# Optimization experiments

Hardware: AMD Instinct MI355X
Metric: run time of the kernel (lower is better)

The kernel has to match this reference:

```python
import jax, jax.numpy as jnp
import numpy as np

SIGMAS = [15, 80, 250]  # hardcoded defaults in retinex_MSR


def _gauss_k1d(sigma):
    # matches get_gauss_kernel(sigma, dim=1)
    ksize = int(np.floor(sigma * 6) / 2) * 2 + 1
    k = np.arange(ksize, dtype=np.float32) - ksize // 2
    k = np.exp(-k ** 2 / (2.0 * sigma ** 2))
    k /= k.sum()
    return jnp.asarray(k)


def _gauss_blur(x, k1d):
    # x: (N, 1, H, W); separable blur with zero padding, same as F.conv2d
    K = k1d.shape[0]
    pad = K // 2
    dn = ('NCHW', 'OIHW', 'NCHW')
    kv = k1d.reshape(1, 1, K, 1)
    kh = k1d.reshape(1, 1, 1, K)
    x = jax.lax.conv_general_dilated(x, kv, (1, 1), [(pad, pad), (0, 0)], dimension_numbers=dn)
    x = jax.lax.conv_general_dilated(x, kh, (1, 1), [(0, 0), (pad, pad)], dimension_numbers=dn)
    return x


def setup_inputs() -> dict:
    key = jax.random.key(0)
    img = jax.random.uniform(key, (16, 3, 512, 512), dtype=jnp.float32)
    return {"img": img}


def reference(img):
    B, C, H, W = img.shape
    # all channels processed identically as single-channel depthwise convs:
    # fold channels into batch for one big conv per sigma
    x = img.astype(jnp.float32).reshape(B * C, 1, H, W)
    w = 1.0 / len(SIGMAS)  # default equal weights summing to 1
    r = jnp.zeros((B * C, 1, H, W), dtype=jnp.float32)
    for sigma in SIGMAS:
        r = r + jnp.log(_gauss_blur(x, _gauss_k1d(sigma)) + 1.0) * w
    r = r.reshape(B, C, H, W)
    # per-channel min-max stretch, global over batch and spatial dims
    mmin = r.min(axis=(0, 2, 3), keepdims=True)
    mmax = r.max(axis=(0, 2, 3), keepdims=True)
    return (r - mmin) / (mmax - mmin)
```

## Files before the change

kernel.cpp:

```cpp
#include <hip/hip_runtime.h>
#include <math.h>


#define NSL 48

#define W0_OFF 0
#define W1_OFF 512
#define W2_OFF 1280
#define MM_OFF 2816
#define G16_BYTE_OFF 16384
#define X16_BYTE_OFF 1589248
#define T16_BYTE_OFF 26755072

typedef _Float16 half8 __attribute__((ext_vector_type(8)));
typedef float f32x4 __attribute__((ext_vector_type(4)));

__device__ __forceinline__ void gload16(const void* g, void* l) {
  __builtin_amdgcn_global_load_lds(
      (const __attribute__((address_space(1))) void*)g,
      (__attribute__((address_space(3))) void*)l, 16, 0, 0);
}

#define WAITV3() asm volatile("s_waitcnt vmcnt(3)" ::: "memory")
#define WAITV0() asm volatile("s_waitcnt vmcnt(0)" ::: "memory")
#define SCHEDB() __builtin_amdgcn_sched_barrier(0)
#define BARRIER() __builtin_amdgcn_s_barrier()

__global__ void wkern(float* __restrict__ ws) {
  __shared__ float red[256];
  const int s = blockIdx.x;
  const int Ks[3] = {91, 481, 1501};
  const float sg[3] = {15.f, 80.f, 250.f};
  const int off[3] = {W0_OFF, W1_OFF, W2_OFF};
  const int alloc[3] = {512, 768, 1536};
  const int K = Ks[s], A = alloc[s];
  float* wb = ws + off[s];
  const int t = threadIdx.x;
  for (int i = t; i < A; i += 256) wb[i] = 0.f;
  __syncthreads();
  const float inv2s2 = 1.f / (2.f * sg[s] * sg[s]);
  float part = 0.f;
  for (int i = t; i < K; i += 256) {
    const float d = (float)(i - K / 2);
    const float e = __expf(-d * d * inv2s2);
    wb[16 + i] = e;
    part += e;
  }
  red[t] = part;
  __syncthreads();
  for (int st = 128; st > 0; st >>= 1) {
    if (t < st) red[t] += red[t + st];
    __syncthreads();
  }
  const float inv = 1.f / red[0];
  for (int i = t; i < K; i += 256) wb[16 + i] *= inv;
}

__global__ void mm_init(unsigned* __restrict__ mm) {
  const int t = threadIdx.x;
  if (t < 3) mm[t] = 0xFFFFFFFFu;
  else if (t < 6) mm[t] = 0u;
}

__global__ void gkern(const float* __restrict__ ws, _Float16* __restrict__ gb) {
  const int y = blockIdx.x;
  const int s = blockIdx.y;
  const int Rs[3] = {45, 240, 750};
  const int off[3] = {W0_OFF, W1_OFF, W2_OFF};
  const float* w = ws + off[s] + 16;
  _Float16* g = gb + ((size_t)s << 18) + ((size_t)y << 9);
  const int R = Rs[s], K = 2 * R + 1;
  for (int x = threadIdx.x; x < 512; x += 256) {
    const int i = x - y + R;
    const float v = (i >= 0 && i < K) ? w[i] : 0.f;
    g[x] = (_Float16)v;
  }
}

__global__ __launch_bounds__(256) void xconv(const float* __restrict__ X,
                                             _Float16* __restrict__ X16) {
  const size_t i = ((size_t)blockIdx.x * 256 + threadIdx.x) << 3;
  const float4 v0 = *reinterpret_cast<const float4*>(X + i);
  const float4 v1 = *reinterpret_cast<const float4*>(X + i + 4);
  half8 h;
  h[0] = (_Float16)v0.x; h[1] = (_Float16)v0.y;
  h[2] = (_Float16)v0.z; h[3] = (_Float16)v0.w;
  h[4] = (_Float16)v1.x; h[5] = (_Float16)v1.y;
  h[6] = (_Float16)v1.z; h[7] = (_Float16)v1.w;
  *reinterpret_cast<half8*>(X16 + i) = h;
}

#define STAGE_P(buf)                                 \
  do {                                               \
    gload16(pA0, &As[buf][t << 3]);                  \
    gload16(pA1, &As[buf][(256 + t) << 3]);          \
    gload16(pB0, &Bs[buf][t << 3]);                  \
    pA0 += 32; pA1 += 32; pB0 += 32;                 \
  } while (0)

#define FRAGS_AND_MFMA(buf)                                                         \
  do {                                                                              \
    half8 af[4], bf[2];                                                             \
    _Pragma("unroll") for (int f = 0; f < 4; ++f)                                   \
        af[f] = *reinterpret_cast<const half8*>(                                    \
            &As[buf][(((wr << 6) + (f << 4) + lr) << 5) + (lg << 3)]);              \
    _Pragma("unroll") for (int f = 0; f < 2; ++f)                                   \
        bf[f] = *reinterpret_cast<const half8*>(                                    \
            &Bs[buf][(((wc << 5) + (f << 4) + lr) << 5) + (lg << 3)]);              \
    _Pragma("unroll") for (int fm = 0; fm < 4; ++fm)                                \
        _Pragma("unroll") for (int fn = 0; fn < 2; ++fn)                            \
        acc[fm][fn] = __builtin_amdgcn_mfma_f32_16x16x32_f16(af[fm], bf[fn],        \
                                                             acc[fm][fn], 0, 0, 0); \
  } while (0)

#define K_PIPELINE_LOOP()                                                           \
  do {                                                                              \
    const _Float16* pA0 =                                                           \
        Ap + ((size_t)(bm + (t >> 2)) << 9) + (klo << 5) + ((t & 3) << 3);          \
    const _Float16* pA1 = pA0 + ((size_t)64 << 9);                                  \
    const _Float16* pB0 =                                                           \
        Bp + ((size_t)(bn + (t >> 2)) << 9) + (klo << 5) + ((t & 3) << 3);          \
    STAGE_P(0);                                                                     \
    STAGE_P(1);                                                                     \
    int cb = 0;                                                                     \
    for (int kt = klo; kt <= khi; ++kt) {                                           \
      if (kt < khi) { WAITV3(); } else { WAITV0(); }                                \
      SCHEDB();                                                                     \
      BARRIER();                                                                    \
      SCHEDB();                                                                     \
      if (kt + 2 <= khi) {                                                          \
        const int sb = (cb + 2 >= 3) ? cb - 1 : cb + 2;                             \
        STAGE_P(sb);                                                                \
      }                                                                             \
      FRAGS_AND_MFMA(cb);                                                           \
      cb = (cb == 2) ? 0 : cb + 1;                                                  \
    }                                                                               \
  } while (0)

__global__ __launch_bounds__(256, 4) void gemm1_k(const _Float16* __restrict__ X16,
                                                  const _Float16* __restrict__ G16,
                                                  _Float16* __restrict__ T16) {
  __shared__ __align__(16) _Float16 As[3][128 * 32];
  __shared__ __align__(16) _Float16 Bs[3][64 * 32];
  const int t = threadIdx.x;
  const int lane = t & 63, wave = t >> 6;
  const int wr = wave >> 1, wc = wave & 1;
  const int lr = lane & 15, lg = lane >> 4;
  const int bn = blockIdx.x << 6;
  const int bm = blockIdx.y << 7;
  const int z = blockIdx.z;
  const int s = z / NSL;
  const int slice = z - s * NSL;
  const int Rs[3] = {45, 240, 750};
  const int R = Rs[s];
  const _Float16* Ap = G16 + ((size_t)s << 18);
  const _Float16* Bp = X16 + ((size_t)slice << 18);
  _Float16* Tout = T16 + ((size_t)z << 18);

  int klo = bm - R;
  klo = (klo > 0 ? klo : 0) >> 5;
  int khi = bm + 127 + R;
  if (khi > 511) khi = 511;
  khi >>= 5;

  f32x4 acc[4][2];
#pragma unroll
  for (int i = 0; i < 4; ++i)
#pragma unroll
    for (int j = 0; j < 2; ++j) acc[i][j] = (f32x4){0.f, 0.f, 0.f, 0.f};

  K_PIPELINE_LOOP();

#pragma unroll
  for (int fm = 0; fm < 4; ++fm)
#pragma unroll
    for (int fn = 0; fn < 2; ++fn) {
      const int a0 = bm + (wr << 6) + (fm << 4) + (lg << 2);
      const int b0 = bn + (wc << 5) + (fn << 4) + lr;
#pragma unroll
      for (int j = 0; j < 4; ++j)
        Tout[((size_t)(a0 + j) << 9) + b0] = (_Float16)acc[fm][fn][j];
    }
}

__global__ __launch_bounds__(256, 3) void gemm2_k(const _Float16* __restrict__ G16,
                                                  const _Float16* __restrict__ T16,
                                                  float* __restrict__ out,
                                                  unsigned* __restrict__ mm) {
  __shared__ __align__(16) _Float16 As[3][128 * 32];
  __shared__ __align__(16) _Float16 Bs[3][64 * 32];
  __shared__ float smn[4], smx[4];
  const int t = threadIdx.x;
  const int lane = t & 63, wave = t >> 6;
  const int wr = wave >> 1, wc = wave & 1;
  const int lr = lane & 15, lg = lane >> 4;
  const int bn = blockIdx.x << 6;
  const int bm = blockIdx.y << 7;
  const int slice = blockIdx.z;
  const float w3 = 1.f / 3.f;
  const int Rs[3] = {45, 240, 750};

  f32x4 res[4][2];
#pragma unroll
  for (int i = 0; i < 4; ++i)
#pragma unroll
    for (int j = 0; j < 2; ++j) res[i][j] = (f32x4){0.f, 0.f, 0.f, 0.f};

#pragma unroll 1
  for (int s = 0; s < 3; ++s) {
    const int R = Rs[s];
    const _Float16* Ap = G16 + ((size_t)s << 18);
    const _Float16* Bp = T16 + ((size_t)(s * NSL + slice) << 18);
    int klo = bm - R;
    klo = (klo > 0 ? klo : 0) >> 5;
    int khi = bm + 127 + R;
    if (khi > 511) khi = 511;
    khi >>= 5;

    f32x4 acc[4][2];
#pragma unroll
    for (int i = 0; i < 4; ++i)
#pragma unroll
      for (int j = 0; j < 2; ++j) acc[i][j] = (f32x4){0.f, 0.f, 0.f, 0.f};

    BARRIER();
    K_PIPELINE_LOOP();

#pragma unroll
    for (int fm = 0; fm < 4; ++fm)
#pragma unroll
      for (int fn = 0; fn < 2; ++fn)
#pragma unroll
        for (int j = 0; j < 4; ++j)
          res[fm][fn][j] += w3 * __logf(acc[fm][fn][j] + 1.f);
  }

  float mn = 3.4e38f, mx = -3.4e38f;
#pragma unroll
  for (int fm = 0; fm < 4; ++fm)
#pragma unroll
    for (int fn = 0; fn < 2; ++fn) {
      const int rb = bm + (wr << 6) + (fm << 4) + (lg << 2);
      const int cg = bn + (wc << 5) + (fn << 4) + lr;
      float* op = out + ((size_t)slice << 18) + ((size_t)rb << 9) + cg;
#pragma unroll
      for (int j = 0; j < 4; ++j) {
        const float v = res[fm][fn][j];
        op[j << 9] = v;
        mn = fminf(mn, v);
        mx = fmaxf(mx, v);
      }
    }
#pragma unroll
  for (int off = 32; off > 0; off >>= 1) {
    mn = fminf(mn, __shfl_xor(mn, off));
    mx = fmaxf(mx, __shfl_xor(mx, off));
  }
  if (lane == 0) {
    smn[wave] = mn;
    smx[wave] = mx;
  }
  __syncthreads();
  if (t == 0) {
    mn = fminf(fminf(smn[0], smn[1]), fminf(smn[2], smn[3]));
    mx = fmaxf(fmaxf(smx[0], smx[1]), fmaxf(smx[2], smx[3]));
    const int ch = slice % 3;
    atomicMin(&mm[ch], __float_as_uint(mn));
    atomicMax(&mm[3 + ch], __float_as_uint(mx));
  }
}

__global__ __launch_bounds__(256) void norm_k(float* __restrict__ r,
                                              const unsigned* __restrict__ mm) {
  const int b = blockIdx.x;
  const int slice = b >> 4;
  const int piece = b & 15;
  const int ch = slice % 3;
  const float mn = __uint_as_float(mm[ch]);
  const float mx = __uint_as_float(mm[3 + ch]);
  const float inv = 1.f / (mx - mn);
  float* p = r + ((size_t)slice << 18) + (piece << 14);
  const int t = threadIdx.x;
  for (int q = 0; q < 16; ++q) {
    float4 v = *reinterpret_cast<const float4*>(&p[(q * 256 + t) << 2]);
    v.x = (v.x - mn) * inv;
    v.y = (v.y - mn) * inv;
    v.z = (v.z - mn) * inv;
    v.w = (v.w - mn) * inv;
    *reinterpret_cast<float4*>(&p[(q * 256 + t) << 2]) = v;
  }
}

extern "C" void kernel_launch(void* const* d_in, const int* in_sizes, int n_in,
                              void* d_out, int out_size, void* d_ws, size_t ws_size,
                              hipStream_t stream) {
  const float* img = (const float*)d_in[0];
  float* out = (float*)d_out;
  float* wsf = (float*)d_ws;
  unsigned* mm = (unsigned*)(wsf + MM_OFF);
  _Float16* G16 = (_Float16*)((char*)d_ws + G16_BYTE_OFF);
  _Float16* X16 = (_Float16*)((char*)d_ws + X16_BYTE_OFF);
  _Float16* T16 = (_Float16*)((char*)d_ws + T16_BYTE_OFF);

  wkern<<<3, 256, 0, stream>>>(wsf);
  mm_init<<<1, 64, 0, stream>>>(mm);
  gkern<<<dim3(512, 3), 256, 0, stream>>>(wsf, G16);
  xconv<<<6144, 256, 0, stream>>>(img, X16);

  gemm1_k<<<dim3(8, 4, 3 * NSL), 256, 0, stream>>>(X16, G16, T16);
  gemm2_k<<<dim3(8, 4, NSL), 256, 0, stream>>>(G16, T16, out, mm);

  norm_k<<<768, 256, 0, stream>>>(out, mm);
}
```

Measured before the change: 171.3 us.

## Preload full swizzled A panel into LDS and widen GEMM tiles to 128x128

Both banded GEMM kernels now load the whole 128x512 fp16 Gaussian-matrix panel into LDS once, using an XOR swizzle, instead of streaming A tiles through a triple buffer. Only B tiles are still pipelined, and they are swizzled too. Blocks grow to 512 threads with 128-wide N tiles, so each block reuses A across twice as many columns, and the wait counts change to match. The ~152KB of LDS per block allows only one block per CU, and the preload fetches all 512 K columns even when the band is narrow. The block-level min/max reduction is replaced by per-wave atomics.

```diff
diff --git a/kernel.cpp b/kernel.cpp
--- a/kernel.cpp
+++ b/kernel.cpp
@@ -21,7 +21,7 @@
       (__attribute__((address_space(3))) void*)l, 16, 0, 0);
 }
 
-#define WAITV3() asm volatile("s_waitcnt vmcnt(3)" ::: "memory")
+#define WAITV1() asm volatile("s_waitcnt vmcnt(1)" ::: "memory")
 #define WAITV0() asm volatile("s_waitcnt vmcnt(0)" ::: "memory")
 #define SCHEDB() __builtin_amdgcn_sched_barrier(0)
 #define BARRIER() __builtin_amdgcn_s_barrier()
@@ -90,23 +90,38 @@
   *reinterpret_cast<half8*>(X16 + i) = h;
 }
 
-#define STAGE_P(buf)                                 \
-  do {                                               \
-    gload16(pA0, &As[buf][t << 3]);                  \
-    gload16(pA1, &As[buf][(256 + t) << 3]);          \
-    gload16(pB0, &Bs[buf][t << 3]);                  \
-    pA0 += 32; pA1 += 32; pB0 += 32;                 \
+#define PRELOAD_A()                                                 \
+  do {                                                              \
+    _Pragma("unroll") for (int i = 0; i < 16; ++i) {                \
+      const int c = (i << 9) + t;                                   \
+      const int row = c >> 6;                                       \
+      const int kc = c & 63;                                        \
+      gload16(Ap + ((size_t)(bm + row) << 9) +                      \
+                  ((kc ^ (row & 7)) << 3),                          \
+              &As[c << 3]);                                         \
+    }                                                               \
   } while (0)
 
-#define FRAGS_AND_MFMA(buf)                                                         \
+#define STAGE_B(buf)                       \
+  do {                                     \
+    gload16(pB, &Bs[buf][t << 3]);         \
+    pB += 32;                              \
+  } while (0)
+
+#define FRAGS_AND_MFMA(buf, kt_)                                                    \
   do {                                                                              \
     half8 af[4], bf[2];                                                             \
-    _Pragma("unroll") for (int f = 0; f < 4; ++f)                                   \
-        af[f] = *reinterpret_cast<const half8*>(                                    \
-            &As[buf][(((wr << 6) + (f << 4) + lr) << 5) + (lg << 3)]);              \
-    _Pragma("unroll") for (int f = 0; f < 2; ++f)                                   \
-        bf[f] = *reinterpret_cast<const half8*>(                                    \
-            &Bs[buf][(((wc << 5) + (f << 4) + lr) << 5) + (lg << 3)]);              \
+    _Pragma("unroll") for (int f = 0; f < 4; ++f) {                                 \
+      const int row = wm + (f << 4) + lr;                                           \
+      const int g = ((kt_) << 2) + lg;                                              \
+      af[f] = *reinterpret_cast<const half8*>(                                      \
+          &As[(row << 9) + ((g ^ (row & 7)) << 3)]);                                \
+    }                                                                               \
+    _Pragma("unroll") for (int f = 0; f < 2; ++f) {                                 \
+      const int n = wn + (f << 4) + lr;                                             \
+      bf[f] = *reinterpret_cast<const half8*>(                                      \
+          &Bs[buf][(n << 5) + ((lg ^ (n & 3)) << 3)]);                              \
+    }                                                                               \
     _Pragma("unroll") for (int fm = 0; fm < 4; ++fm)                                \
         _Pragma("unroll") for (int fn = 0; fn < 2; ++fn)                            \
         acc[fm][fn] = __builtin_amdgcn_mfma_f32_16x16x32_f16(af[fm], bf[fn],        \
@@ -115,38 +130,38 @@
 
 #define K_PIPELINE_LOOP()                                                           \
   do {                                                                              \
-    const _Float16* pA0 =                                                           \
-        Ap + ((size_t)(bm + (t >> 2)) << 9) + (klo << 5) + ((t & 3) << 3);          \
-    const _Float16* pA1 = pA0 + ((size_t)64 << 9);                                  \
-    const _Float16* pB0 =                                                           \
-        Bp + ((size_t)(bn + (t >> 2)) << 9) + (klo << 5) + ((t & 3) << 3);          \
-    STAGE_P(0);                                                                     \
-    STAGE_P(1);                                                                     \
+    PRELOAD_A();                                                                    \
+    const int nrow_ = t >> 2;                                                       \
+    const int kc4_ = t & 3;                                                         \
+    const _Float16* pB = Bp + ((size_t)(bn + nrow_) << 9) + (klo << 5) +            \
+                         ((kc4_ ^ (nrow_ & 3)) << 3);                               \
+    STAGE_B(0);                                                                     \
+    STAGE_B(1);                                                                     \
     int cb = 0;                                                                     \
     for (int kt = klo; kt <= khi; ++kt) {                                           \
-      if (kt < khi) { WAITV3(); } else { WAITV0(); }                                \
+      if (kt < khi) { WAITV1(); } else { WAITV0(); }                                \
       SCHEDB();                                                                     \
       BARRIER();                                                                    \
       SCHEDB();                                                                     \
       if (kt + 2 <= khi) {                                                          \
         const int sb = (cb + 2 >= 3) ? cb - 1 : cb + 2;                             \
-        STAGE_P(sb);                                                                \
+        STAGE_B(sb);                                                                \
       }                                                                             \
-      FRAGS_AND_MFMA(cb);                                                           \
+      FRAGS_AND_MFMA(cb, kt);                                                       \
       cb = (cb == 2) ? 0 : cb + 1;                                                  \
     }                                                                               \
   } while (0)
 
-__global__ __launch_bounds__(256, 4) void gemm1_k(const _Float16* __restrict__ X16,
+__global__ __launch_bounds__(512, 2) void gemm1_k(const _Float16* __restrict__ X16,
                                                   const _Float16* __restrict__ G16,
                                                   _Float16* __restrict__ T16) {
-  __shared__ __align__(16) _Float16 As[3][128 * 32];
-  __shared__ __align__(16) _Float16 Bs[3][64 * 32];
+  __shared__ __align__(16) _Float16 As[128 * 512];
+  __shared__ __align__(16) _Float16 Bs[3][128 * 32];
   const int t = threadIdx.x;
   const int lane = t & 63, wave = t >> 6;
-  const int wr = wave >> 1, wc = wave & 1;
+  const int wm = (wave >> 2) << 6, wn = (wave & 3) << 5;
   const int lr = lane & 15, lg = lane >> 4;
-  const int bn = blockIdx.x << 6;
+  const int bn = blockIdx.x << 7;
   const int bm = blockIdx.y << 7;
   const int z = blockIdx.z;
   const int s = z / NSL;
@@ -175,26 +190,25 @@
   for (int fm = 0; fm < 4; ++fm)
 #pragma unroll
     for (int fn = 0; fn < 2; ++fn) {
-      const int a0 = bm + (wr << 6) + (fm << 4) + (lg << 2);
-      const int b0 = bn + (wc << 5) + (fn << 4) + lr;
+      const int a0 = bm + wm + (fm << 4) + (lg << 2);
+      const int b0 = bn + wn + (fn << 4) + lr;
 #pragma unroll
       for (int j = 0; j < 4; ++j)
         Tout[((size_t)(a0 + j) << 9) + b0] = (_Float16)acc[fm][fn][j];
     }
 }
 
-__global__ __launch_bounds__(256, 3) void gemm2_k(const _Float16* __restrict__ G16,
+__global__ __launch_bounds__(512, 2) void gemm2_k(const _Float16* __restrict__ G16,
                                                   const _Float16* __restrict__ T16,
                                                   float* __restrict__ out,
                                                   unsigned* __restrict__ mm) {
-  __shared__ __align__(16) _Float16 As[3][128 * 32];
-  __shared__ __align__(16) _Float16 Bs[3][64 * 32];
-  __shared__ float smn[4], smx[4];
+  __shared__ __align__(16) _Float16 As[128 * 512];
+  __shared__ __align__(16) _Float16 Bs[3][128 * 32];
   const int t = threadIdx.x;
   const int lane = t & 63, wave = t >> 6;
-  const int wr = wave >> 1, wc = wave & 1;
+  const int wm = (wave >> 2) << 6, wn = (wave & 3) << 5;
   const int lr = lane & 15, lg = lane >> 4;
-  const int bn = blockIdx.x << 6;
+  const int bn = blockIdx.x << 7;
   const int bm = blockIdx.y << 7;
   const int slice = blockIdx.z;
   const float w3 = 1.f / 3.f;
@@ -223,7 +237,7 @@
 #pragma unroll
       for (int j = 0; j < 2; ++j) acc[i][j] = (f32x4){0.f, 0.f, 0.f, 0.f};
 
-    BARRIER();
+    if (s > 0) BARRIER();
     K_PIPELINE_LOOP();
 
 #pragma unroll
@@ -240,8 +254,8 @@
   for (int fm = 0; fm < 4; ++fm)
 #pragma unroll
     for (int fn = 0; fn < 2; ++fn) {
-      const int rb = bm + (wr << 6) + (fm << 4) + (lg << 2);
-      const int cg = bn + (wc << 5) + (fn << 4) + lr;
+      const int rb = bm + wm + (fm << 4) + (lg << 2);
+      const int cg = bn + wn + (fn << 4) + lr;
       float* op = out + ((size_t)slice << 18) + ((size_t)rb << 9) + cg;
 #pragma unroll
       for (int j = 0; j < 4; ++j) {
@@ -257,13 +271,6 @@
     mx = fmaxf(mx, __shfl_xor(mx, off));
   }
   if (lane == 0) {
-    smn[wave] = mn;
-    smx[wave] = mx;
-  }
-  __syncthreads();
-  if (t == 0) {
-    mn = fminf(fminf(smn[0], smn[1]), fminf(smn[2], smn[3]));
-    mx = fmaxf(fmaxf(smx[0], smx[1]), fmaxf(smx[2], smx[3]));
     const int ch = slice % 3;
     atomicMin(&mm[ch], __float_as_uint(mn));
     atomicMax(&mm[3 + ch], __float_as_uint(mx));
@@ -307,8 +314,8 @@
   gkern<<<dim3(512, 3), 256, 0, stream>>>(wsf, G16);
   xconv<<<6144, 256, 0, stream>>>(img, X16);
 
-  gemm1_k<<<dim3(8, 4, 3 * NSL), 256, 0, stream>>>(X16, G16, T16);
-  gemm2_k<<<dim3(8, 4, NSL), 256, 0, stream>>>(G16, T16, out, mm);
+  gemm1_k<<<dim3(4, 4, 3 * NSL), 512, 0, stream>>>(X16, G16, T16);
+  gemm2_k<<<dim3(4, 4, NSL), 512, 0, stream>>>(G16, T16, out, mm);
 
   norm_k<<<768, 256, 0, stream>>>(out, mm);
 }
```

Measured after the change: 306.3 us. 1.79x slower.
